# Kernel tuning notes

Measured on AMD Instinct MI355X. Metric: run time of the kernel, lower is better.

Reference implementation:

```python
import jax, jax.numpy as jnp
import numpy as np

B, N, F = 32, 1024, 7
HID, HID_GLO, MLP_H, OUT = 256, 8, 64, 8
THRESHOLD = 0.3


def setup_inputs() -> dict:
    key = jax.random.key(0)
    ks = jax.random.split(key, 16)
    def lin(k, fan_out, fan_in):
        # xavier-uniform-like init
        lim = (6.0 / (fan_in + fan_out)) ** 0.5
        return jax.random.uniform(k, (fan_out, fan_in), jnp.float32, -lim, lim)
    return {
        "x": jax.random.normal(ks[0], (B, N, F), jnp.float32),
        "W1": lin(ks[1], HID, 2),   "b1": jnp.zeros((HID,), jnp.float32),
        "W2": lin(ks[2], HID, HID), "b2": jnp.zeros((HID,), jnp.float32),
        "Wfc": lin(ks[3], HID, HID), "bfc": jnp.zeros((HID,), jnp.float32),
        "Wg": lin(ks[4], HID_GLO, 2), "bg": jnp.zeros((HID_GLO,), jnp.float32),
        "Wm0": lin(ks[5], MLP_H, N * F), "bm0": jnp.zeros((MLP_H,), jnp.float32),
        "Wm1": lin(ks[6], MLP_H, MLP_H), "bm1": jnp.zeros((MLP_H,), jnp.float32),
        "Wp": lin(ks[7], OUT, MLP_H + HID + HID_GLO), "bp": jnp.zeros((OUT,), jnp.float32),
    }


def reference(x, W1, b1, W2, b2, Wfc, bfc, Wg, bg, Wm0, bm0, Wm1, bm1, Wp, bp):
    # --- GCN branch (torch code detaches node features & adjacency) ---
    pts = jax.lax.stop_gradient(x[:, :, 1:3])                     # [B,N,2]
    diff = pts[:, :, None, :] - pts[:, None, :, :]                # [B,N,N,2]
    dist = jnp.sqrt(jnp.sum(diff * diff, axis=-1))                # [B,N,N]
    adj = (dist < THRESHOLD).astype(x.dtype)                      # [B,N,N]
    dinv = 1.0 / jnp.sqrt(jnp.sum(adj, axis=-1))                  # [B,N] (>=1, self-loop)
    nadj = dinv[:, :, None] * adj * dinv[:, None, :]              # D^-1/2 A D^-1/2
    h = jax.nn.relu(jnp.einsum('bij,bjd->bid', nadj, pts) @ W1.T + b1)   # [B,N,256]
    g = jnp.einsum('bij,bjh->bih', nadj, h) @ W2.T + b2                  # [B,N,256]
    gcn_en = jnp.mean(g, axis=1) @ Wfc.T + bfc                    # [B,256]

    # --- global branch (torch code uses .item() -> constants) ---
    v = jax.lax.stop_gradient(x[:, :, 1:5])                       # [B,N,4]
    avg_speed = jnp.mean(jnp.linalg.norm(v[:, :, 2:4], axis=-1), axis=1)  # [B]
    density = 1.0 / jnp.max(dist, axis=(1, 2))                    # [B] (v3 == pts)
    glo_in = jnp.stack([avg_speed, density], axis=-1)             # [B,2]
    glo_en = jax.nn.relu(glo_in @ Wg.T + bg)                      # [B,8]

    # --- MLP branch on flattened x ---
    xf = x.reshape(x.shape[0], -1)                                # [B, N*F]
    xf = jax.nn.relu(xf @ Wm0.T + bm0)
    xf = jax.nn.relu(xf @ Wm1.T + bm1)                            # [B,64]

    out = jnp.concatenate([xf, gcn_en, glo_en], axis=1) @ Wp.T + bp  # [B,8]
    return out
```

## Files before the change

kernel.cpp:

```cpp
#include <hip/hip_runtime.h>

#define BB 32
#define NN 1024
#define FF 7
#define HID 256
#define MLPH 64
#define OUTN 8
#define CATN (MLPH + HID + 8)

__device__ __forceinline__ float wave_sum(float v) {
#pragma unroll
    for (int m = 32; m >= 1; m >>= 1) v += __shfl_xor(v, m, 64);
    return v;
}
__device__ __forceinline__ float wave_max(float v) {
#pragma unroll
    for (int m = 32; m >= 1; m >>= 1) v = fmaxf(v, __shfl_xor(v, m, 64));
    return v;
}

__global__ __launch_bounds__(1024, 4) void kPM(const float* __restrict__ x,
                                               const float* __restrict__ Wm0,
                                               const float* __restrict__ W2,
                                               const float* __restrict__ b2,
                                               const float* __restrict__ Wfc,
                                               const float* __restrict__ bfc,
                                               const float* __restrict__ Wp,
                                               float* __restrict__ pts0,
                                               float* __restrict__ pts1,
                                               float* __restrict__ spd,
                                               float* __restrict__ mlp_p,
                                               float* __restrict__ E,
                                               float* __restrict__ cE) {
    __shared__ __align__(16) float sbuf[NN * FF];
    __shared__ float wred[16];
    int blk = blockIdx.x, tid = threadIdx.x, lane = tid & 63, w = tid >> 6;
    if (blk < 32) {
        int b = blk;
        const float4* xr = (const float4*)(x + b * (NN * FF));
        float4* s4 = (float4*)sbuf;
        for (int i = tid; i < 1792; i += 1024) s4[i] = xr[i];
        __syncthreads();
        pts0[b * NN + tid] = sbuf[tid * FF + 1];
        pts1[b * NN + tid] = sbuf[tid * FF + 2];
        float vx = sbuf[tid * FF + 3], vy = sbuf[tid * FF + 4];
        float sp = sqrtf(fmaf(vx, vx, vy * vy));
        sp = wave_sum(sp);
        if (lane == 0) wred[w] = sp;
        __syncthreads();
        if (tid == 0) {
            float s = 0.f;
#pragma unroll
            for (int i = 0; i < 16; ++i) s += wred[i];
            spd[b] = s;
        }
    } else if (blk < 40) {
        int o = blk - 32;
        float* l0 = sbuf;
        float* l1 = sbuf + 256;
        float* r2 = sbuf + 512;
        if (tid < HID) l0[tid] = Wp[o * CATN + MLPH + tid];
        __syncthreads();
        if (tid < HID) {
            float a = 0.f;
#pragma unroll 8
            for (int m = 0; m < HID; ++m) a = fmaf(l0[m], Wfc[m * HID + tid], a);
            l1[tid] = a;
            r2[tid] = l0[tid] * bfc[tid];
        }
        __syncthreads();
        if (tid < HID) {
            float e = 0.f;
#pragma unroll 8
            for (int k = 0; k < HID; ++k) e = fmaf(l1[k], W2[k * HID + tid], e);
            E[o * HID + tid] = e;
            float c = fmaf(l1[tid], b2[tid], r2[tid]);
            c = wave_sum(c);
            if (lane == 0) wred[w] = c;
        }
        __syncthreads();
        if (tid == 0) cE[o] = wred[0] + wred[1] + wred[2] + wred[3];
    } else {
        int h = blk - 40;
        const float4* wr = (const float4*)(Wm0 + h * (NN * FF));
        float4* s4 = (float4*)sbuf;
        for (int i = tid; i < 1792; i += 1024) s4[i] = wr[i];
        __syncthreads();
#pragma unroll
        for (int rep = 0; rep < 2; ++rep) {
            int b = w * 2 + rep;
            const float4* xr = (const float4*)(x + b * (NN * FF));
            float4 a4 = {0.f, 0.f, 0.f, 0.f};
#pragma unroll 7
            for (int it = 0; it < 28; ++it) {
                float4 xv = xr[it * 64 + lane];
                float4 wv = s4[it * 64 + lane];
                a4.x = fmaf(wv.x, xv.x, a4.x);
                a4.y = fmaf(wv.y, xv.y, a4.y);
                a4.z = fmaf(wv.z, xv.z, a4.z);
                a4.w = fmaf(wv.w, xv.w, a4.w);
            }
            float s = (a4.x + a4.y) + (a4.z + a4.w);
            s = wave_sum(s);
            if (lane == 0) mlp_p[b * MLPH + h] = s;
        }
    }
}

__global__ __launch_bounds__(1024, 4) void kA(const float* __restrict__ pts0,
                                              const float* __restrict__ pts1,
                                              float* __restrict__ deg,
                                              float* __restrict__ bmaxp) {
    __shared__ __align__(16) float l0[NN];
    __shared__ __align__(16) float l1[NN];
    __shared__ __align__(16) float s2[NN];
    __shared__ __align__(16) float s3[NN];
    __shared__ float wred[16];
    int blk = blockIdx.x, tid = threadIdx.x, lane = tid & 63, w = tid >> 6;
    int b = blk >> 3, jg = blk & 7;
    l0[tid] = pts0[b * NN + tid];
    l1[tid] = pts1[b * NN + tid];
    __syncthreads();
    int jA = jg * 128 + lane, jB = jA + 64;
    float pj0a = l0[jA], pj1a = l1[jA];
    float pj0b = l0[jB], pj1b = l1[jB];
    const float4* v0p = (const float4*)&l0[w * 64];
    const float4* v1p = (const float4*)&l1[w * 64];
    unsigned dA = 0u, dB = 0u;
    float mx = 0.f;
#pragma unroll 4
    for (int g = 0; g < 16; ++g) {
        float4 v0 = v0p[g], v1 = v1p[g];
        float dx, dy, d2a, d2b;
        dx = pj0a - v0.x; dy = pj1a - v1.x; d2a = fmaf(dy, dy, dx * dx);
        dx = pj0b - v0.x; dy = pj1b - v1.x; d2b = fmaf(dy, dy, dx * dx);
        dA += (d2a <= 0.09f); dB += (d2b <= 0.09f);
        mx = fmaxf(mx, fmaxf(d2a, d2b));
        dx = pj0a - v0.y; dy = pj1a - v1.y; d2a = fmaf(dy, dy, dx * dx);
        dx = pj0b - v0.y; dy = pj1b - v1.y; d2b = fmaf(dy, dy, dx * dx);
        dA += (d2a <= 0.09f); dB += (d2b <= 0.09f);
        mx = fmaxf(mx, fmaxf(d2a, d2b));
        dx = pj0a - v0.z; dy = pj1a - v1.z; d2a = fmaf(dy, dy, dx * dx);
        dx = pj0b - v0.z; dy = pj1b - v1.z; d2b = fmaf(dy, dy, dx * dx);
        dA += (d2a <= 0.09f); dB += (d2b <= 0.09f);
        mx = fmaxf(mx, fmaxf(d2a, d2b));
        dx = pj0a - v0.w; dy = pj1a - v1.w; d2a = fmaf(dy, dy, dx * dx);
        dx = pj0b - v0.w; dy = pj1b - v1.w; d2b = fmaf(dy, dy, dx * dx);
        dA += (d2a <= 0.09f); dB += (d2b <= 0.09f);
        mx = fmaxf(mx, fmaxf(d2a, d2b));
    }
    s2[tid] = (float)dA;
    s3[tid] = (float)dB;
    mx = wave_max(mx);
    if (lane == 0) wred[w] = mx;
    __syncthreads();
    if (tid < 64) {
        float s = 0.f;
#pragma unroll
        for (int kk = 0; kk < 16; ++kk) s += s2[kk * 64 + tid];
        deg[b * NN + jg * 128 + tid] = s;
    } else if (tid < 128) {
        int t = tid - 64;
        float s = 0.f;
#pragma unroll
        for (int kk = 0; kk < 16; ++kk) s += s3[kk * 64 + t];
        deg[b * NN + jg * 128 + 64 + t] = s;
    }
    if (tid == 0) {
        float m = wred[0];
#pragma unroll
        for (int i = 1; i < 16; ++i) m = fmaxf(m, wred[i]);
        bmaxp[b * 8 + jg] = m;
    }
}

__global__ __launch_bounds__(1024, 4) void kB(const float* __restrict__ pts0,
                                              const float* __restrict__ pts1,
                                              const float* __restrict__ deg,
                                              float* __restrict__ q0,
                                              float* __restrict__ q1,
                                              float* __restrict__ wj) {
    __shared__ __align__(16) float l0[NN];
    __shared__ __align__(16) float l1[NN];
    __shared__ __align__(16) float di[NN];
    __shared__ __align__(16) float r0a[NN];
    __shared__ __align__(16) float r1a[NN];
    __shared__ __align__(16) float r2a[NN];
    __shared__ __align__(16) float r0b[NN];
    __shared__ __align__(16) float r1b[NN];
    __shared__ __align__(16) float r2b[NN];
    int blk = blockIdx.x, tid = threadIdx.x, lane = tid & 63, w = tid >> 6;
    int b = blk >> 3, jg = blk & 7;
    l0[tid] = pts0[b * NN + tid];
    l1[tid] = pts1[b * NN + tid];
    di[tid] = 1.0f / sqrtf(deg[b * NN + tid]);
    __syncthreads();
    int jA = jg * 128 + lane, jB = jA + 64;
    float pj0a = l0[jA], pj1a = l1[jA];
    float pj0b = l0[jB], pj1b = l1[jB];
    const float4* v0p = (const float4*)&l0[w * 64];
    const float4* v1p = (const float4*)&l1[w * 64];
    const float4* vdp = (const float4*)&di[w * 64];
    float a0a = 0.f, a1a = 0.f, asa = 0.f;
    float a0b = 0.f, a1b = 0.f, asb = 0.f;
#pragma unroll 4
    for (int g = 0; g < 16; ++g) {
        float4 v0 = v0p[g], v1 = v1p[g], vd = vdp[g];
        float dx, dy, d2, t;
        dx = pj0a - v0.x; dy = pj1a - v1.x; d2 = fmaf(dy, dy, dx * dx);
        t = (d2 <= 0.09f) ? vd.x : 0.0f;
        a0a = fmaf(t, v0.x, a0a); a1a = fmaf(t, v1.x, a1a); asa += t;
        dx = pj0b - v0.x; dy = pj1b - v1.x; d2 = fmaf(dy, dy, dx * dx);
        t = (d2 <= 0.09f) ? vd.x : 0.0f;
        a0b = fmaf(t, v0.x, a0b); a1b = fmaf(t, v1.x, a1b); asb += t;
        dx = pj0a - v0.y; dy = pj1a - v1.y; d2 = fmaf(dy, dy, dx * dx);
        t = (d2 <= 0.09f) ? vd.y : 0.0f;
        a0a = fmaf(t, v0.y, a0a); a1a = fmaf(t, v1.y, a1a); asa += t;
        dx = pj0b - v0.y; dy = pj1b - v1.y; d2 = fmaf(dy, dy, dx * dx);
        t = (d2 <= 0.09f) ? vd.y : 0.0f;
        a0b = fmaf(t, v0.y, a0b); a1b = fmaf(t, v1.y, a1b); asb += t;
        dx = pj0a - v0.z; dy = pj1a - v1.z; d2 = fmaf(dy, dy, dx * dx);
        t = (d2 <= 0.09f) ? vd.z : 0.0f;
        a0a = fmaf(t, v0.z, a0a); a1a = fmaf(t, v1.z, a1a); asa += t;
        dx = pj0b - v0.z; dy = pj1b - v1.z; d2 = fmaf(dy, dy, dx * dx);
        t = (d2 <= 0.09f) ? vd.z : 0.0f;
        a0b = fmaf(t, v0.z, a0b); a1b = fmaf(t, v1.z, a1b); asb += t;
        dx = pj0a - v0.w; dy = pj1a - v1.w; d2 = fmaf(dy, dy, dx * dx);
        t = (d2 <= 0.09f) ? vd.w : 0.0f;
        a0a = fmaf(t, v0.w, a0a); a1a = fmaf(t, v1.w, a1a); asa += t;
        dx = pj0b - v0.w; dy = pj1b - v1.w; d2 = fmaf(dy, dy, dx * dx);
        t = (d2 <= 0.09f) ? vd.w : 0.0f;
        a0b = fmaf(t, v0.w, a0b); a1b = fmaf(t, v1.w, a1b); asb += t;
    }
    r0a[tid] = a0a; r1a[tid] = a1a; r2a[tid] = asa;
    r0b[tid] = a0b; r1b[tid] = a1b; r2b[tid] = asb;
    __syncthreads();
    if (tid < 128) {
        int t = tid & 63;
        const float* R0 = (tid < 64) ? r0a : r0b;
        const float* R1 = (tid < 64) ? r1a : r1b;
        const float* R2 = (tid < 64) ? r2a : r2b;
        int j = jg * 128 + ((tid < 64) ? 0 : 64) + t;
        float s0 = 0.f, s1 = 0.f, ss = 0.f;
#pragma unroll
        for (int kk = 0; kk < 16; ++kk) {
            s0 += R0[kk * 64 + t];
            s1 += R1[kk * 64 + t];
            ss += R2[kk * 64 + t];
        }
        float dj = di[j];
        q0[b * NN + j] = dj * s0;
        q1[b * NN + j] = dj * s1;
        wj[b * NN + j] = dj * ss * (1.0f / NN);
    }
}

__global__ __launch_bounds__(1024, 4) void kF(const float* __restrict__ q0,
                                              const float* __restrict__ q1,
                                              const float* __restrict__ wj,
                                              const float* __restrict__ W1,
                                              const float* __restrict__ b1,
                                              const float* __restrict__ Wg,
                                              const float* __restrict__ bg,
                                              const float* __restrict__ Wm1,
                                              const float* __restrict__ bm1,
                                              const float* __restrict__ Wp,
                                              const float* __restrict__ bp,
                                              const float* __restrict__ bm0,
                                              const float* __restrict__ mlp_p,
                                              const float* __restrict__ bmaxp,
                                              const float* __restrict__ spd,
                                              const float* __restrict__ E,
                                              const float* __restrict__ cE,
                                              float* __restrict__ out) {
    __shared__ __align__(16) float sq0[NN];
    __shared__ __align__(16) float sq1[NN];
    __shared__ __align__(16) float sw[NN];
    __shared__ __align__(16) float hpp[4][HID];
    __shared__ __align__(16) float hs[HID];
    __shared__ float sx1[MLPH];
    __shared__ float sxf2[MLPH];
    __shared__ float sglo[8];
    int b = blockIdx.x, tid = threadIdx.x;
    sq0[tid] = q0[b * NN + tid];
    sq1[tid] = q1[b * NN + tid];
    sw[tid]  = wj[b * NN + tid];
    if (tid >= 448 && tid < 512) {
        int h = tid - 448;
        sx1[h] = fmaxf(mlp_p[b * MLPH + h] + bm0[h], 0.f);
    }
    __syncthreads();
    {
        int h = tid & 255, jq = tid >> 8;
        float w10 = W1[h * 2], w11 = W1[h * 2 + 1], bb = b1[h];
        float acc = 0.f;
        const float4* q0v4 = (const float4*)&sq0[jq * 256];
        const float4* q1v4 = (const float4*)&sq1[jq * 256];
        const float4* wv4  = (const float4*)&sw[jq * 256];
#pragma unroll 4
        for (int g = 0; g < 64; ++g) {
            float4 q0v = q0v4[g], q1v = q1v4[g], wv = wv4[g];
            acc = fmaf(wv.x, fmaxf(fmaf(q1v.x, w11, fmaf(q0v.x, w10, bb)), 0.f), acc);
            acc = fmaf(wv.y, fmaxf(fmaf(q1v.y, w11, fmaf(q0v.y, w10, bb)), 0.f), acc);
            acc = fmaf(wv.z, fmaxf(fmaf(q1v.z, w11, fmaf(q0v.z, w10, bb)), 0.f), acc);
            acc = fmaf(wv.w, fmaxf(fmaf(q1v.w, w11, fmaf(q0v.w, w10, bb)), 0.f), acc);
        }
        hpp[jq][h] = acc;
    }
    __syncthreads();
    if (tid < HID) {
        hs[tid] = hpp[0][tid] + hpp[1][tid] + hpp[2][tid] + hpp[3][tid];
    } else if (tid < HID + MLPH) {
        int t = tid - HID;
        float a = bm1[t];
        const float* wv = Wm1 + t * MLPH;
#pragma unroll
        for (int k = 0; k < MLPH; ++k) a = fmaf(wv[k], sx1[k], a);
        sxf2[t] = fmaxf(a, 0.f);
    } else if (tid < HID + MLPH + 8) {
        int t = tid - HID - MLPH;
        float mx = 0.f;
#pragma unroll
        for (int g = 0; g < 8; ++g) mx = fmaxf(mx, bmaxp[b * 8 + g]);
        float avg  = spd[b] * (1.0f / NN);
        float dens = 1.0f / sqrtf(mx);
        sglo[t] = fmaxf(fmaf(Wg[t * 2], avg, fmaf(Wg[t * 2 + 1], dens, bg[t])), 0.f);
    }
    __syncthreads();
    if (tid < 512) {
        int o = tid >> 6, lane = tid & 63;
        const float* Eo = E + o * HID;
        float a = Eo[lane] * hs[lane];
        a = fmaf(Eo[lane + 64],  hs[lane + 64],  a);
        a = fmaf(Eo[lane + 128], hs[lane + 128], a);
        a = fmaf(Eo[lane + 192], hs[lane + 192], a);
        a = fmaf(Wp[o * CATN + lane], sxf2[lane], a);
        a = wave_sum(a);
        if (lane == 0) {
            const float* wg = Wp + o * CATN + MLPH + HID;
#pragma unroll
            for (int g = 0; g < 8; ++g) a = fmaf(wg[g], sglo[g], a);
            out[b * OUTN + o] = a + cE[o] + bp[o];
        }
    }
}

extern "C" void kernel_launch(void* const* d_in, const int* in_sizes, int n_in,
                              void* d_out, int out_size, void* d_ws, size_t ws_size,
                              hipStream_t stream) {
    const float* x   = (const float*)d_in[0];
    const float* W1  = (const float*)d_in[1];
    const float* b1  = (const float*)d_in[2];
    const float* W2  = (const float*)d_in[3];
    const float* b2  = (const float*)d_in[4];
    const float* Wfc = (const float*)d_in[5];
    const float* bfc = (const float*)d_in[6];
    const float* Wg  = (const float*)d_in[7];
    const float* bg  = (const float*)d_in[8];
    const float* Wm0 = (const float*)d_in[9];
    const float* bm0 = (const float*)d_in[10];
    const float* Wm1 = (const float*)d_in[11];
    const float* bm1 = (const float*)d_in[12];
    const float* Wp  = (const float*)d_in[13];
    const float* bp  = (const float*)d_in[14];
    float* out = (float*)d_out;
    float* ws  = (float*)d_ws;

    float* pts0  = ws;
    float* pts1  = ws + 32768;
    float* deg   = ws + 65536;
    float* q0    = ws + 98304;
    float* q1    = ws + 131072;
    float* wj    = ws + 163840;
    float* mlp_p = ws + 196608;
    float* bmaxp = ws + 198656;
    float* spd   = ws + 198912;
    float* E     = ws + 198944;
    float* cE    = ws + 200992;

    kPM<<<104, 1024, 0, stream>>>(x, Wm0, W2, b2, Wfc, bfc, Wp,
                                  pts0, pts1, spd, mlp_p, E, cE);
    kA<<<256,  1024, 0, stream>>>(pts0, pts1, deg, bmaxp);
    kB<<<256,  1024, 0, stream>>>(pts0, pts1, deg, q0, q1, wj);
    kF<<<BB,   1024, 0, stream>>>(q0, q1, wj, W1, b1, Wg, bg, Wm1, bm1, Wp, bp,
                                  bm0, mlp_p, bmaxp, spd, E, cE, out);
}
```

Baseline: 130.8 us.

## Fuse four kernels into two with a last-block atomic reduction for the final stage

After: 210.3 us. 1.61x slower.

```diff
diff --git a/kernel.cpp b/kernel.cpp
--- a/kernel.cpp
+++ b/kernel.cpp
@@ -19,188 +19,201 @@
     return v;
 }
 
-__global__ __launch_bounds__(1024, 4) void kPM(const float* __restrict__ x,
-                                               const float* __restrict__ Wm0,
-                                               const float* __restrict__ W2,
-                                               const float* __restrict__ b2,
-                                               const float* __restrict__ Wfc,
-                                               const float* __restrict__ bfc,
-                                               const float* __restrict__ Wp,
-                                               float* __restrict__ pts0,
-                                               float* __restrict__ pts1,
-                                               float* __restrict__ spd,
-                                               float* __restrict__ mlp_p,
-                                               float* __restrict__ E,
-                                               float* __restrict__ cE) {
-    __shared__ __align__(16) float sbuf[NN * FF];
-    __shared__ float wred[16];
+union S1 {
+    struct { float xb[NN * FF]; float l0[NN], l1[NN], s2[NN], s3[NN]; float wred[16]; } a;
+    struct { float xb[NN * FF]; float wred[16]; } p;
+    struct { float l0[HID], l1[HID], r2[HID]; float wred[16]; } c;
+    struct { float wb[NN * FF]; } m;
+};
+
+__global__ __launch_bounds__(1024, 4) void k1(const float* __restrict__ x,
+                                              const float* __restrict__ Wm0,
+                                              const float* __restrict__ W2,
+                                              const float* __restrict__ b2,
+                                              const float* __restrict__ Wfc,
+                                              const float* __restrict__ bfc,
+                                              const float* __restrict__ Wp,
+                                              float* __restrict__ pts0,
+                                              float* __restrict__ pts1,
+                                              float* __restrict__ spd,
+                                              float* __restrict__ mlp_p,
+                                              float* __restrict__ E,
+                                              float* __restrict__ cE,
+                                              float* __restrict__ deg,
+                                              float* __restrict__ bmaxp,
+                                              int* __restrict__ done) {
+    __shared__ __align__(16) S1 sm;
     int blk = blockIdx.x, tid = threadIdx.x, lane = tid & 63, w = tid >> 6;
-    if (blk < 32) {
-        int b = blk;
+    if (blk < 256) {
+        int b = blk >> 3, jg = blk & 7;
         const float4* xr = (const float4*)(x + b * (NN * FF));
-        float4* s4 = (float4*)sbuf;
+        float4* s4 = (float4*)sm.a.xb;
         for (int i = tid; i < 1792; i += 1024) s4[i] = xr[i];
         __syncthreads();
-        pts0[b * NN + tid] = sbuf[tid * FF + 1];
-        pts1[b * NN + tid] = sbuf[tid * FF + 2];
-        float vx = sbuf[tid * FF + 3], vy = sbuf[tid * FF + 4];
+        sm.a.l0[tid] = sm.a.xb[tid * FF + 1];
+        sm.a.l1[tid] = sm.a.xb[tid * FF + 2];
+        __syncthreads();
+        int jA = jg * 128 + lane, jB = jA + 64;
+        float pj0a = sm.a.l0[jA], pj1a = sm.a.l1[jA];
+        float pj0b = sm.a.l0[jB], pj1b = sm.a.l1[jB];
+        const float4* v0p = (const float4*)&sm.a.l0[w * 64];
+        const float4* v1p = (const float4*)&sm.a.l1[w * 64];
+        unsigned dA = 0u, dB = 0u;
+        float mx = 0.f;
+#pragma unroll 4
+        for (int g = 0; g < 16; ++g) {
+            float4 v0 = v0p[g], v1 = v1p[g];
+            float dx, dy, d2a, d2b;
+            dx = pj0a - v0.x; dy = pj1a - v1.x; d2a = fmaf(dy, dy, dx * dx);
+            dx = pj0b - v0.x; dy = pj1b - v1.x; d2b = fmaf(dy, dy, dx * dx);
+            dA += (d2a <= 0.09f); dB += (d2b <= 0.09f);
+            mx = fmaxf(mx, fmaxf(d2a, d2b));
+            dx = pj0a - v0.y; dy = pj1a - v1.y; d2a = fmaf(dy, dy, dx * dx);
+            dx = pj0b - v0.y; dy = pj1b - v1.y; d2b = fmaf(dy, dy, dx * dx);
+            dA += (d2a <= 0.09f); dB += (d2b <= 0.09f);
+            mx = fmaxf(mx, fmaxf(d2a, d2b));
+            dx = pj0a - v0.z; dy = pj1a - v1.z; d2a = fmaf(dy, dy, dx * dx);
+            dx = pj0b - v0.z; dy = pj1b - v1.z; d2b = fmaf(dy, dy, dx * dx);
+            dA += (d2a <= 0.09f); dB += (d2b <= 0.09f);
+            mx = fmaxf(mx, fmaxf(d2a, d2b));
+            dx = pj0a - v0.w; dy = pj1a - v1.w; d2a = fmaf(dy, dy, dx * dx);
+            dx = pj0b - v0.w; dy = pj1b - v1.w; d2b = fmaf(dy, dy, dx * dx);
+            dA += (d2a <= 0.09f); dB += (d2b <= 0.09f);
+            mx = fmaxf(mx, fmaxf(d2a, d2b));
+        }
+        sm.a.s2[tid] = (float)dA;
+        sm.a.s3[tid] = (float)dB;
+        mx = wave_max(mx);
+        if (lane == 0) sm.a.wred[w] = mx;
+        __syncthreads();
+        if (tid < 64) {
+            float s = 0.f;
+#pragma unroll
+            for (int kk = 0; kk < 16; ++kk) s += sm.a.s2[kk * 64 + tid];
+            deg[b * NN + jg * 128 + tid] = s;
+        } else if (tid < 128) {
+            int t = tid - 64;
+            float s = 0.f;
+#pragma unroll
+            for (int kk = 0; kk < 16; ++kk) s += sm.a.s3[kk * 64 + t];
+            deg[b * NN + jg * 128 + 64 + t] = s;
+        }
+        if (tid == 0) {
+            float m = sm.a.wred[0];
+#pragma unroll
+            for (int i = 1; i < 16; ++i) m = fmaxf(m, sm.a.wred[i]);
+            bmaxp[b * 8 + jg] = m;
+        }
+    } else if (blk < 288) {
+        int b = blk - 256;
+        const float4* xr = (const float4*)(x + b * (NN * FF));
+        float4* s4 = (float4*)sm.p.xb;
+        for (int i = tid; i < 1792; i += 1024) s4[i] = xr[i];
+        __syncthreads();
+        pts0[b * NN + tid] = sm.p.xb[tid * FF + 1];
+        pts1[b * NN + tid] = sm.p.xb[tid * FF + 2];
+        float vx = sm.p.xb[tid * FF + 3], vy = sm.p.xb[tid * FF + 4];
         float sp = sqrtf(fmaf(vx, vx, vy * vy));
         sp = wave_sum(sp);
-        if (lane == 0) wred[w] = sp;
+        if (lane == 0) sm.p.wred[w] = sp;
         __syncthreads();
         if (tid == 0) {
             float s = 0.f;
 #pragma unroll
-            for (int i = 0; i < 16; ++i) s += wred[i];
+            for (int i = 0; i < 16; ++i) s += sm.p.wred[i];
             spd[b] = s;
-        }
-    } else if (blk < 40) {
-        int o = blk - 32;
-        float* l0 = sbuf;
-        float* l1 = sbuf + 256;
-        float* r2 = sbuf + 512;
-        if (tid < HID) l0[tid] = Wp[o * CATN + MLPH + tid];
+            done[b] = 0;
+        }
+    } else if (blk < 296) {
+        int o = blk - 288;
+        if (tid < HID) sm.c.l0[tid] = Wp[o * CATN + MLPH + tid];
         __syncthreads();
         if (tid < HID) {
             float a = 0.f;
 #pragma unroll 8
-            for (int m = 0; m < HID; ++m) a = fmaf(l0[m], Wfc[m * HID + tid], a);
-            l1[tid] = a;
-            r2[tid] = l0[tid] * bfc[tid];
+            for (int m = 0; m < HID; ++m) a = fmaf(sm.c.l0[m], Wfc[m * HID + tid], a);
+            sm.c.l1[tid] = a;
+            sm.c.r2[tid] = sm.c.l0[tid] * bfc[tid];
         }
         __syncthreads();
         if (tid < HID) {
             float e = 0.f;
 #pragma unroll 8
-            for (int k = 0; k < HID; ++k) e = fmaf(l1[k], W2[k * HID + tid], e);
+            for (int k = 0; k < HID; ++k) e = fmaf(sm.c.l1[k], W2[k * HID + tid], e);
             E[o * HID + tid] = e;
-            float c = fmaf(l1[tid], b2[tid], r2[tid]);
+            float c = fmaf(sm.c.l1[tid], b2[tid], sm.c.r2[tid]);
             c = wave_sum(c);
-            if (lane == 0) wred[w] = c;
-        }
-        __syncthreads();
-        if (tid == 0) cE[o] = wred[0] + wred[1] + wred[2] + wred[3];
+            if (lane == 0) sm.c.wred[w] = c;
+        }
+        __syncthreads();
+        if (tid == 0) cE[o] = sm.c.wred[0] + sm.c.wred[1] + sm.c.wred[2] + sm.c.wred[3];
     } else {
-        int h = blk - 40;
+        int t = blk - 296, h = t >> 1, half = t & 1;
         const float4* wr = (const float4*)(Wm0 + h * (NN * FF));
-        float4* s4 = (float4*)sbuf;
+        float4* s4 = (float4*)sm.m.wb;
         for (int i = tid; i < 1792; i += 1024) s4[i] = wr[i];
         __syncthreads();
-#pragma unroll
-        for (int rep = 0; rep < 2; ++rep) {
-            int b = w * 2 + rep;
-            const float4* xr = (const float4*)(x + b * (NN * FF));
-            float4 a4 = {0.f, 0.f, 0.f, 0.f};
+        int b = half * 16 + w;
+        const float4* xr = (const float4*)(x + b * (NN * FF));
+        float4 a4 = {0.f, 0.f, 0.f, 0.f};
 #pragma unroll 7
-            for (int it = 0; it < 28; ++it) {
-                float4 xv = xr[it * 64 + lane];
-                float4 wv = s4[it * 64 + lane];
-                a4.x = fmaf(wv.x, xv.x, a4.x);
-                a4.y = fmaf(wv.y, xv.y, a4.y);
-                a4.z = fmaf(wv.z, xv.z, a4.z);
-                a4.w = fmaf(wv.w, xv.w, a4.w);
-            }
-            float s = (a4.x + a4.y) + (a4.z + a4.w);
-            s = wave_sum(s);
-            if (lane == 0) mlp_p[b * MLPH + h] = s;
-        }
-    }
-}
-
-__global__ __launch_bounds__(1024, 4) void kA(const float* __restrict__ pts0,
+        for (int it = 0; it < 28; ++it) {
+            float4 xv = xr[it * 64 + lane];
+            float4 wv = s4[it * 64 + lane];
+            a4.x = fmaf(wv.x, xv.x, a4.x);
+            a4.y = fmaf(wv.y, xv.y, a4.y);
+            a4.z = fmaf(wv.z, xv.z, a4.z);
+            a4.w = fmaf(wv.w, xv.w, a4.w);
+        }
+        float s = (a4.x + a4.y) + (a4.z + a4.w);
+        s = wave_sum(s);
+        if (lane == 0) mlp_p[b * MLPH + h] = s;
+    }
+}
+
+union S2 {
+    struct {
+        float l0[NN], l1[NN], di[NN];
+        float r0a[NN], r1a[NN], r2a[NN], r0b[NN], r1b[NN], r2b[NN];
+        float q0[128], q1[128], qw[128];
+    } b;
+    struct { float hs[HID]; float sx1[MLPH]; float sxf2[MLPH]; float sglo[8]; } f;
+};
+
+__global__ __launch_bounds__(1024, 4) void k2(const float* __restrict__ pts0,
                                               const float* __restrict__ pts1,
-                                              float* __restrict__ deg,
-                                              float* __restrict__ bmaxp) {
-    __shared__ __align__(16) float l0[NN];
-    __shared__ __align__(16) float l1[NN];
-    __shared__ __align__(16) float s2[NN];
-    __shared__ __align__(16) float s3[NN];
-    __shared__ float wred[16];
+                                              const float* __restrict__ deg,
+                                              const float* __restrict__ W1,
+                                              const float* __restrict__ b1,
+                                              const float* __restrict__ Wg,
+                                              const float* __restrict__ bg,
+                                              const float* __restrict__ Wm1,
+                                              const float* __restrict__ bm1,
+                                              const float* __restrict__ Wp,
+                                              const float* __restrict__ bp,
+                                              const float* __restrict__ bm0,
+                                              const float* __restrict__ mlp_p,
+                                              const float* __restrict__ bmaxp,
+                                              const float* __restrict__ spd,
+                                              const float* __restrict__ E,
+                                              const float* __restrict__ cE,
+                                              float* __restrict__ hpart,
+                                              int* __restrict__ done,
+                                              float* __restrict__ out) {
+    __shared__ __align__(16) S2 sm;
+    __shared__ int lastflag;
     int blk = blockIdx.x, tid = threadIdx.x, lane = tid & 63, w = tid >> 6;
     int b = blk >> 3, jg = blk & 7;
-    l0[tid] = pts0[b * NN + tid];
-    l1[tid] = pts1[b * NN + tid];
+    sm.b.l0[tid] = pts0[b * NN + tid];
+    sm.b.l1[tid] = pts1[b * NN + tid];
+    sm.b.di[tid] = 1.0f / sqrtf(deg[b * NN + tid]);
     __syncthreads();
     int jA = jg * 128 + lane, jB = jA + 64;
-    float pj0a = l0[jA], pj1a = l1[jA];
-    float pj0b = l0[jB], pj1b = l1[jB];
-    const float4* v0p = (const float4*)&l0[w * 64];
-    const float4* v1p = (const float4*)&l1[w * 64];
-    unsigned dA = 0u, dB = 0u;
-    float mx = 0.f;
-#pragma unroll 4
-    for (int g = 0; g < 16; ++g) {
-        float4 v0 = v0p[g], v1 = v1p[g];
-        float dx, dy, d2a, d2b;
-        dx = pj0a - v0.x; dy = pj1a - v1.x; d2a = fmaf(dy, dy, dx * dx);
-        dx = pj0b - v0.x; dy = pj1b - v1.x; d2b = fmaf(dy, dy, dx * dx);
-        dA += (d2a <= 0.09f); dB += (d2b <= 0.09f);
-        mx = fmaxf(mx, fmaxf(d2a, d2b));
-        dx = pj0a - v0.y; dy = pj1a - v1.y; d2a = fmaf(dy, dy, dx * dx);
-        dx = pj0b - v0.y; dy = pj1b - v1.y; d2b = fmaf(dy, dy, dx * dx);
-        dA += (d2a <= 0.09f); dB += (d2b <= 0.09f);
-        mx = fmaxf(mx, fmaxf(d2a, d2b));
-        dx = pj0a - v0.z; dy = pj1a - v1.z; d2a = fmaf(dy, dy, dx * dx);
-        dx = pj0b - v0.z; dy = pj1b - v1.z; d2b = fmaf(dy, dy, dx * dx);
-        dA += (d2a <= 0.09f); dB += (d2b <= 0.09f);
-        mx = fmaxf(mx, fmaxf(d2a, d2b));
-        dx = pj0a - v0.w; dy = pj1a - v1.w; d2a = fmaf(dy, dy, dx * dx);
-        dx = pj0b - v0.w; dy = pj1b - v1.w; d2b = fmaf(dy, dy, dx * dx);
-        dA += (d2a <= 0.09f); dB += (d2b <= 0.09f);
-        mx = fmaxf(mx, fmaxf(d2a, d2b));
-    }
-    s2[tid] = (float)dA;
-    s3[tid] = (float)dB;
-    mx = wave_max(mx);
-    if (lane == 0) wred[w] = mx;
-    __syncthreads();
-    if (tid < 64) {
-        float s = 0.f;
-#pragma unroll
-        for (int kk = 0; kk < 16; ++kk) s += s2[kk * 64 + tid];
-        deg[b * NN + jg * 128 + tid] = s;
-    } else if (tid < 128) {
-        int t = tid - 64;
-        float s = 0.f;
-#pragma unroll
-        for (int kk = 0; kk < 16; ++kk) s += s3[kk * 64 + t];
-        deg[b * NN + jg * 128 + 64 + t] = s;
-    }
-    if (tid == 0) {
-        float m = wred[0];
-#pragma unroll
-        for (int i = 1; i < 16; ++i) m = fmaxf(m, wred[i]);
-        bmaxp[b * 8 + jg] = m;
-    }
-}
-
-__global__ __launch_bounds__(1024, 4) void kB(const float* __restrict__ pts0,
-                                              const float* __restrict__ pts1,
-                                              const float* __restrict__ deg,
-                                              float* __restrict__ q0,
-                                              float* __restrict__ q1,
-                                              float* __restrict__ wj) {
-    __shared__ __align__(16) float l0[NN];
-    __shared__ __align__(16) float l1[NN];
-    __shared__ __align__(16) float di[NN];
-    __shared__ __align__(16) float r0a[NN];
-    __shared__ __align__(16) float r1a[NN];
-    __shared__ __align__(16) float r2a[NN];
-    __shared__ __align__(16) float r0b[NN];
-    __shared__ __align__(16) float r1b[NN];
-    __shared__ __align__(16) float r2b[NN];
-    int blk = blockIdx.x, tid = threadIdx.x, lane = tid & 63, w = tid >> 6;
-    int b = blk >> 3, jg = blk & 7;
-    l0[tid] = pts0[b * NN + tid];
-    l1[tid] = pts1[b * NN + tid];
-    di[tid] = 1.0f / sqrtf(deg[b * NN + tid]);
-    __syncthreads();
-    int jA = jg * 128 + lane, jB = jA + 64;
-    float pj0a = l0[jA], pj1a = l1[jA];
-    float pj0b = l0[jB], pj1b = l1[jB];
-    const float4* v0p = (const float4*)&l0[w * 64];
-    const float4* v1p = (const float4*)&l1[w * 64];
-    const float4* vdp = (const float4*)&di[w * 64];
+    float pj0a = sm.b.l0[jA], pj1a = sm.b.l1[jA];
+    float pj0b = sm.b.l0[jB], pj1b = sm.b.l1[jB];
+    const float4* v0p = (const float4*)&sm.b.l0[w * 64];
+    const float4* v1p = (const float4*)&sm.b.l1[w * 64];
+    const float4* vdp = (const float4*)&sm.b.di[w * 64];
     float a0a = 0.f, a1a = 0.f, asa = 0.f;
     float a0b = 0.f, a1b = 0.f, asb = 0.f;
 #pragma unroll 4
@@ -232,15 +245,15 @@
         t = (d2 <= 0.09f) ? vd.w : 0.0f;
         a0b = fmaf(t, v0.w, a0b); a1b = fmaf(t, v1.w, a1b); asb += t;
     }
-    r0a[tid] = a0a; r1a[tid] = a1a; r2a[tid] = asa;
-    r0b[tid] = a0b; r1b[tid] = a1b; r2b[tid] = asb;
+    sm.b.r0a[tid] = a0a; sm.b.r1a[tid] = a1a; sm.b.r2a[tid] = asa;
+    sm.b.r0b[tid] = a0b; sm.b.r1b[tid] = a1b; sm.b.r2b[tid] = asb;
     __syncthreads();
     if (tid < 128) {
         int t = tid & 63;
-        const float* R0 = (tid < 64) ? r0a : r0b;
-        const float* R1 = (tid < 64) ? r1a : r1b;
-        const float* R2 = (tid < 64) ? r2a : r2b;
-        int j = jg * 128 + ((tid < 64) ? 0 : 64) + t;
+        const float* R0 = (tid < 64) ? sm.b.r0a : sm.b.r0b;
+        const float* R1 = (tid < 64) ? sm.b.r1a : sm.b.r1b;
+        const float* R2 = (tid < 64) ? sm.b.r2a : sm.b.r2b;
+        int j = jg * 128 + tid;
         float s0 = 0.f, s1 = 0.f, ss = 0.f;
 #pragma unroll
         for (int kk = 0; kk < 16; ++kk) {
@@ -248,99 +261,81 @@
             s1 += R1[kk * 64 + t];
             ss += R2[kk * 64 + t];
         }
-        float dj = di[j];
-        q0[b * NN + j] = dj * s0;
-        q1[b * NN + j] = dj * s1;
-        wj[b * NN + j] = dj * ss * (1.0f / NN);
-    }
-}
-
-__global__ __launch_bounds__(1024, 4) void kF(const float* __restrict__ q0,
-                                              const float* __restrict__ q1,
-                                              const float* __restrict__ wj,
-                                              const float* __restrict__ W1,
-                                              const float* __restrict__ b1,
-                                              const float* __restrict__ Wg,
-                                              const float* __restrict__ bg,
-                                              const float* __restrict__ Wm1,
-                                              const float* __restrict__ bm1,
-                                              const float* __restrict__ Wp,
-                                              const float* __restrict__ bp,
-                                              const float* __restrict__ bm0,
-                                              const float* __restrict__ mlp_p,
-                                              const float* __restrict__ bmaxp,
-                                              const float* __restrict__ spd,
-                                              const float* __restrict__ E,
-                                              const float* __restrict__ cE,
-                                              float* __restrict__ out) {
-    __shared__ __align__(16) float sq0[NN];
-    __shared__ __align__(16) float sq1[NN];
-    __shared__ __align__(16) float sw[NN];
-    __shared__ __align__(16) float hpp[4][HID];
-    __shared__ __align__(16) float hs[HID];
-    __shared__ float sx1[MLPH];
-    __shared__ float sxf2[MLPH];
-    __shared__ float sglo[8];
-    int b = blockIdx.x, tid = threadIdx.x;
-    sq0[tid] = q0[b * NN + tid];
-    sq1[tid] = q1[b * NN + tid];
-    sw[tid]  = wj[b * NN + tid];
-    if (tid >= 448 && tid < 512) {
-        int h = tid - 448;
-        sx1[h] = fmaxf(mlp_p[b * MLPH + h] + bm0[h], 0.f);
+        float dj = sm.b.di[j];
+        sm.b.q0[tid] = dj * s0;
+        sm.b.q1[tid] = dj * s1;
+        sm.b.qw[tid] = dj * ss * (1.0f / NN);
     }
     __syncthreads();
     {
         int h = tid & 255, jq = tid >> 8;
-        float w10 = W1[h * 2], w11 = W1[h * 2 + 1], bb = b1[h];
+        float w10 = W1[2 * h], w11 = W1[2 * h + 1], bb = b1[h];
+        const float4* q0v = (const float4*)&sm.b.q0[jq * 32];
+        const float4* q1v = (const float4*)&sm.b.q1[jq * 32];
+        const float4* qwv = (const float4*)&sm.b.qw[jq * 32];
         float acc = 0.f;
-        const float4* q0v4 = (const float4*)&sq0[jq * 256];
-        const float4* q1v4 = (const float4*)&sq1[jq * 256];
-        const float4* wv4  = (const float4*)&sw[jq * 256];
-#pragma unroll 4
-        for (int g = 0; g < 64; ++g) {
-            float4 q0v = q0v4[g], q1v = q1v4[g], wv = wv4[g];
-            acc = fmaf(wv.x, fmaxf(fmaf(q1v.x, w11, fmaf(q0v.x, w10, bb)), 0.f), acc);
-            acc = fmaf(wv.y, fmaxf(fmaf(q1v.y, w11, fmaf(q0v.y, w10, bb)), 0.f), acc);
-            acc = fmaf(wv.z, fmaxf(fmaf(q1v.z, w11, fmaf(q0v.z, w10, bb)), 0.f), acc);
-            acc = fmaf(wv.w, fmaxf(fmaf(q1v.w, w11, fmaf(q0v.w, w10, bb)), 0.f), acc);
-        }
-        hpp[jq][h] = acc;
+#pragma unroll
+        for (int g = 0; g < 8; ++g) {
+            float4 qa = q0v[g], qb = q1v[g], qw4 = qwv[g];
+            acc = fmaf(qw4.x, fmaxf(fmaf(qb.x, w11, fmaf(qa.x, w10, bb)), 0.f), acc);
+            acc = fmaf(qw4.y, fmaxf(fmaf(qb.y, w11, fmaf(qa.y, w10, bb)), 0.f), acc);
+            acc = fmaf(qw4.z, fmaxf(fmaf(qb.z, w11, fmaf(qa.z, w10, bb)), 0.f), acc);
+            acc = fmaf(qw4.w, fmaxf(fmaf(qb.w, w11, fmaf(qa.w, w10, bb)), 0.f), acc);
+        }
+        sm.b.r0a[jq * 256 + h] = acc;
     }
     __syncthreads();
     if (tid < HID) {
-        hs[tid] = hpp[0][tid] + hpp[1][tid] + hpp[2][tid] + hpp[3][tid];
+        float s = sm.b.r0a[tid] + sm.b.r0a[256 + tid] + sm.b.r0a[512 + tid] + sm.b.r0a[768 + tid];
+        hpart[(b * 8 + jg) * HID + tid] = s;
+    }
+    __threadfence();
+    __syncthreads();
+    if (tid == 0) lastflag = (atomicAdd(&done[b], 1) == 7);
+    __syncthreads();
+    if (!lastflag) return;
+    __threadfence();
+    if (tid < HID) {
+        float s = 0.f;
+#pragma unroll
+        for (int g = 0; g < 8; ++g) s += hpart[(b * 8 + g) * HID + tid];
+        sm.f.hs[tid] = s;
     } else if (tid < HID + MLPH) {
-        int t = tid - HID;
-        float a = bm1[t];
-        const float* wv = Wm1 + t * MLPH;
-#pragma unroll
-        for (int k = 0; k < MLPH; ++k) a = fmaf(wv[k], sx1[k], a);
-        sxf2[t] = fmaxf(a, 0.f);
+        int t2 = tid - HID;
+        sm.f.sx1[t2] = fmaxf(mlp_p[b * MLPH + t2] + bm0[t2], 0.f);
     } else if (tid < HID + MLPH + 8) {
-        int t = tid - HID - MLPH;
+        int t2 = tid - HID - MLPH;
         float mx = 0.f;
 #pragma unroll
         for (int g = 0; g < 8; ++g) mx = fmaxf(mx, bmaxp[b * 8 + g]);
         float avg  = spd[b] * (1.0f / NN);
         float dens = 1.0f / sqrtf(mx);
-        sglo[t] = fmaxf(fmaf(Wg[t * 2], avg, fmaf(Wg[t * 2 + 1], dens, bg[t])), 0.f);
+        sm.f.sglo[t2] = fmaxf(fmaf(Wg[t2 * 2], avg, fmaf(Wg[t2 * 2 + 1], dens, bg[t2])), 0.f);
+    }
+    __syncthreads();
+    if (tid < MLPH) {
+        float a = bm1[tid];
+        const float* wv = Wm1 + tid * MLPH;
+#pragma unroll
+        for (int k = 0; k < MLPH; ++k) a = fmaf(wv[k], sm.f.sx1[k], a);
+        sm.f.sxf2[tid] = fmaxf(a, 0.f);
     }
     __syncthreads();
     if (tid < 512) {
-        int o = tid >> 6, lane = tid & 63;
+        int o = tid >> 6, ln = tid & 63;
         const float* Eo = E + o * HID;
-        float a = Eo[lane] * hs[lane];
-        a = fmaf(Eo[lane + 64],  hs[lane + 64],  a);
-        a = fmaf(Eo[lane + 128], hs[lane + 128], a);
-        a = fmaf(Eo[lane + 192], hs[lane + 192], a);
-        a = fmaf(Wp[o * CATN + lane], sxf2[lane], a);
+        float a = Eo[ln] * sm.f.hs[ln];
+        a = fmaf(Eo[ln + 64],  sm.f.hs[ln + 64],  a);
+        a = fmaf(Eo[ln + 128], sm.f.hs[ln + 128], a);
+        a = fmaf(Eo[ln + 192], sm.f.hs[ln + 192], a);
+        a = fmaf(Wp[o * CATN + ln], sm.f.sxf2[ln], a);
         a = wave_sum(a);
-        if (lane == 0) {
+        if (ln == 0) {
             const float* wg = Wp + o * CATN + MLPH + HID;
-#pragma unroll
-            for (int g = 0; g < 8; ++g) a = fmaf(wg[g], sglo[g], a);
-            out[b * OUTN + o] = a + cE[o] + bp[o];
+            float r = a;
+#pragma unroll
+            for (int g = 0; g < 8; ++g) r = fmaf(wg[g], sm.f.sglo[g], r);
+            out[b * OUTN + o] = r + cE[o] + bp[o];
         }
     }
 }
@@ -369,19 +364,17 @@
     float* pts0  = ws;
     float* pts1  = ws + 32768;
     float* deg   = ws + 65536;
-    float* q0    = ws + 98304;
-    float* q1    = ws + 131072;
-    float* wj    = ws + 163840;
-    float* mlp_p = ws + 196608;
-    float* bmaxp = ws + 198656;
-    float* spd   = ws + 198912;
-    float* E     = ws + 198944;
-    float* cE    = ws + 200992;
-
-    kPM<<<104, 1024, 0, stream>>>(x, Wm0, W2, b2, Wfc, bfc, Wp,
-                                  pts0, pts1, spd, mlp_p, E, cE);
-    kA<<<256,  1024, 0, stream>>>(pts0, pts1, deg, bmaxp);
-    kB<<<256,  1024, 0, stream>>>(pts0, pts1, deg, q0, q1, wj);
-    kF<<<BB,   1024, 0, stream>>>(q0, q1, wj, W1, b1, Wg, bg, Wm1, bm1, Wp, bp,
-                                  bm0, mlp_p, bmaxp, spd, E, cE, out);
-}
+    float* mlp_p = ws + 98304;
+    float* bmaxp = ws + 100352;
+    float* spd   = ws + 100608;
+    float* E     = ws + 100640;
+    float* cE    = ws + 102688;
+    int*   done  = (int*)(ws + 102720);
+    float* hpart = ws + 102752;
+
+    k1<<<424, 1024, 0, stream>>>(x, Wm0, W2, b2, Wfc, bfc, Wp,
+                                 pts0, pts1, spd, mlp_p, E, cE, deg, bmaxp, done);
+    k2<<<256, 1024, 0, stream>>>(pts0, pts1, deg, W1, b1, Wg, bg, Wm1, bm1,
+                                 Wp, bp, bm0, mlp_p, bmaxp, spd, E, cE,
+                                 hpart, done, out);
+}
```
